# Performance work log

Hardware: AMD Instinct MI355X
Metric: run time of the kernel (lower is better)

## Reference

```python
import jax, jax.numpy as jnp
import numpy as np


def setup_inputs() -> dict:
    key = jax.random.key(0)
    k1, k2 = jax.random.split(key)
    BATCH, NUM_PROBES, DIM = 2048, 512, 256
    X = jax.random.uniform(k1, (BATCH, DIM), dtype=jnp.float32)
    probes = jax.random.uniform(k2, (NUM_PROBES, DIM), dtype=jnp.float32)
    return {"X": X, "probes": probes}


def reference(X, probes):
    # Godel implication a -> b: 1.0 if a <= b else b, applied on the
    # broadcast [batch, num_probes, dim] grid, then mean over dim.
    Xe = X[:, None, :]            # [B, 1, D]
    Pe = probes[None, :, :]       # [1, P, D]
    implication = jnp.where(Pe <= Xe, jnp.float32(1.0), Xe)  # [B, P, D]
    return implication.mean(axis=-1)  # [B, P]
```

## Files before the change

### kernel.cpp

```cpp
#include <hip/hip_runtime.h>
#include <stdint.h>


#define BATCH  2048
#define NPROBE 512
#define DIM    256

typedef float f4 __attribute__((ext_vector_type(4)));
typedef float f2 __attribute__((ext_vector_type(2)));

__global__ __launch_bounds__(1024, 4)
void yoneda_kernel(const float* __restrict__ X, const float* __restrict__ Pr,
                   float* __restrict__ out) {
  __shared__ float lds[32768];

  const int tid = threadIdx.x;
  const int b0 = blockIdx.y * 64, p0 = blockIdx.x * 64;
  const float K = 16777216.0f;

  #pragma unroll
  for (int s = 0; s < 4; ++s) {
    int idx = s * 1024 + tid;
    int r = idx >> 6, q = idx & 63;
    int slot = (q & 56) | ((q ^ r) & 7);
    f4 xv = *(const f4*)(X  + (size_t)(b0 + r) * DIM + 4 * q);
    f4 pv = *(const f4*)(Pr + (size_t)(p0 + r) * DIM + 4 * q);
    f4 yv, qv;
    #pragma unroll
    for (int e = 0; e < 4; ++e) {
      yv[e] = 1.0f - xv[e];
      qv[e] = __builtin_fmaf(pv[e], -K, K) + 1.0f;
    }
    *(f4*)&lds[r * 256 + 4 * slot]         = yv;
    *(f4*)&lds[16384 + r * 256 + 4 * slot] = qv;
  }

  const int wv   = tid >> 6;
  const int g2   = wv >> 1;
  const int ph   = wv & 1;
  const int gtid = tid & 63;
  const int tb   = gtid >> 3;
  const int tp   = gtid & 7;

  int xrow[8], prow[4];
  #pragma unroll
  for (int i = 0; i < 8; ++i) xrow[i] = (tb + 8 * i) * 256 + g2 * 32;
  #pragma unroll
  for (int j = 0; j < 4; ++j) prow[j] = 16384 + (ph * 32 + tp + 8 * j) * 256 + g2 * 32;

  f2 acc2[8][4], accy2[8];
  #pragma unroll
  for (int i = 0; i < 8; ++i) {
    accy2[i] = (f2){0.0f, 0.0f};
    #pragma unroll
    for (int j = 0; j < 4; ++j) acc2[i][j] = (f2){0.0f, 0.0f};
  }
  const f2 mK2 = {-K, -K};

  __syncthreads();

  #pragma unroll 1
  for (int s = 0; s < 8; ++s) {
    const int xo = 4 * (s ^ tb);
    const int po = 4 * (s ^ tp);
    f4 pv[4];
    #pragma unroll
    for (int j = 0; j < 4; ++j) pv[j] = *(const f4*)&lds[prow[j] + po];
    #pragma unroll
    for (int i = 0; i < 8; ++i) {
      f4 yv = *(const f4*)&lds[xrow[i] + xo];
      f2 ya = {yv[0], yv[1]}, yc = {yv[2], yv[3]};
      accy2[i] += ya;
      accy2[i] += yc;
      #pragma unroll
      for (int j = 0; j < 4; ++j) {
        f2 pa = {pv[j][0], pv[j][1]}, pc = {pv[j][2], pv[j][3]};
        f2 ma, mc;
        asm("v_pk_fma_f32 %0, %1, %2, %3 clamp"
            : "=v"(ma) : "v"(ya), "v"(mK2), "v"(pa));
        asm("v_pk_fma_f32 %0, %1, %2, %0"
            : "+v"(acc2[i][j]) : "v"(ma), "v"(ya));
        asm("v_pk_fma_f32 %0, %1, %2, %3 clamp"
            : "=v"(mc) : "v"(yc), "v"(mK2), "v"(pc));
        asm("v_pk_fma_f32 %0, %1, %2, %0"
            : "+v"(acc2[i][j]) : "v"(mc), "v"(yc));
      }
    }
  }

  __syncthreads();
  const int tbx   = tb << 2;
  const int obase = tb * 64 + ph * 32 + tp;
  const int gseg  = g2 << 12;
  #pragma unroll
  for (int i = 0; i < 8; ++i) {
    float sxg = 32.0f - (accy2[i][0] + accy2[i][1]);
    #pragma unroll
    for (int j = 0; j < 4; ++j) {
      int o = obase + 512 * i + 8 * j;
      lds[gseg + (o ^ tbx)] = sxg + acc2[i][j][0] + acc2[i][j][1];
    }
  }
  __syncthreads();
  const float inv  = 1.0f / 256.0f;
  const int   fold = ((tid >> 5) & 7) << 2;
  #pragma unroll
  for (int k = 0; k < 2; ++k) {
    int o = 2 * (k * 1024 + tid);
    int a = o ^ fold;
    f2 v = *(const f2*)&lds[a];
    #pragma unroll
    for (int g = 1; g < 8; ++g)
      v += *(const f2*)&lds[(g << 12) + a];
    v *= inv;
    int row = o >> 6, col = o & 63;
    *(f2*)&out[(size_t)(b0 + row) * NPROBE + p0 + col] = v;
  }
}

extern "C" void kernel_launch(void* const* d_in, const int* in_sizes, int n_in,
                              void* d_out, int out_size, void* d_ws, size_t ws_size,
                              hipStream_t stream) {
  const float* X  = (const float*)d_in[0];
  const float* Pr = (const float*)d_in[1];
  float* outp = (float*)d_out;
  dim3 grid(NPROBE / 64, BATCH / 64);
  yoneda_kernel<<<grid, 1024, 0, stream>>>(X, Pr, outp);
}
```

Baseline: 22.07 us.

## Split into prep kernel and main kernel using scalar-broadcast probe operands

```diff
diff --git a/kernel.cpp b/kernel.cpp
--- a/kernel.cpp
+++ b/kernel.cpp
@@ -9,15 +9,113 @@
 typedef float f4 __attribute__((ext_vector_type(4)));
 typedef float f2 __attribute__((ext_vector_type(2)));
 
+#define KF 16777216.0f
+#define Q1_OFF 0
+#define SX_OFF (NPROBE * DIM)
+#define WS_NEED ((size_t)((SX_OFF + BATCH) * 4))
+
+__global__ __launch_bounds__(512)
+void prep_kernel(const float* __restrict__ X, const float* __restrict__ Pr,
+                 float* __restrict__ ws) {
+  const int wv   = blockIdx.x * 8 + (threadIdx.x >> 6);
+  const int lane = threadIdx.x & 63;
+  if (wv < BATCH) {
+    f4 v = *(const f4*)(X + (size_t)wv * DIM + 4 * lane);
+    float s = (v[0] + v[1]) + (v[2] + v[3]);
+    #pragma unroll
+    for (int off = 32; off; off >>= 1) s += __shfl_xor(s, off, 64);
+    if (lane == 0) ws[SX_OFF + wv] = s;
+  } else {
+    const int p = wv - BATCH;
+    f4 v = *(const f4*)(Pr + (size_t)p * DIM + 4 * lane);
+    f4 q;
+    #pragma unroll
+    for (int e = 0; e < 4; ++e)
+      q[e] = __builtin_fmaf(v[e], -KF, KF) + 1.0f;
+    *(f4*)(ws + Q1_OFF + (size_t)p * DIM + 4 * lane) = q;
+  }
+}
+
+__global__ __launch_bounds__(512, 2)
+void yoneda_main(const float* __restrict__ X, const float* __restrict__ ws,
+                 float* __restrict__ out) {
+  __shared__ float yl[64 * 260];
+
+  const int tid = threadIdx.x;
+  const int p0  = blockIdx.x * 64;
+  const int b0  = blockIdx.y * 64;
+
+  #pragma unroll
+  for (int s = 0; s < 8; ++s) {
+    int idx = s * 512 + tid;
+    int r = idx >> 6, c = idx & 63;
+    f4 v = *(const f4*)(X + (size_t)(b0 + r) * DIM + 4 * c);
+    f4 y;
+    #pragma unroll
+    for (int e = 0; e < 4; ++e) y[e] = 1.0f - v[e];
+    *(f4*)&yl[r * 260 + 4 * c] = y;
+  }
+
+  const int w = __builtin_amdgcn_readfirstlane(tid >> 6);
+  const int l = tid & 63;
+  const float* q1w = ws + Q1_OFF + (size_t)(p0 + w * 8) * DIM;
+  const float sxv  = ws[SX_OFF + b0 + l];
+
+  f2 acc[8];
+  #pragma unroll
+  for (int j = 0; j < 8; ++j) acc[j] = (f2){0.0f, 0.0f};
+  const f2 mK2 = {-KF, -KF};
+
+  __syncthreads();
+
+  #pragma unroll 1
+  for (int dc = 0; dc < 4; ++dc) {
+    f4 yq[16];
+    #pragma unroll
+    for (int i = 0; i < 16; ++i)
+      yq[i] = *(const f4*)&yl[l * 260 + dc * 64 + 4 * i];
+    #pragma unroll
+    for (int jj = 0; jj < 8; ++jj) {
+      const f2* q2p = (const f2*)(q1w + jj * DIM + dc * 64);
+      #pragma unroll
+      for (int u = 0; u < 32; ++u) {
+        f2 q2 = q2p[u];
+        f2 y2 = (u & 1) ? (f2){yq[u >> 1][2], yq[u >> 1][3]}
+                        : (f2){yq[u >> 1][0], yq[u >> 1][1]};
+        f2 m;
+        asm("v_pk_fma_f32 %0, %1, %2, %3 clamp"
+            : "=v"(m) : "v"(y2), "v"(mK2), "s"(q2));
+        asm("v_pk_fma_f32 %0, %1, %2, %0"
+            : "+v"(acc[jj]) : "v"(m), "v"(y2));
+      }
+    }
+  }
+
+  __syncthreads();
+  #pragma unroll
+  for (int jj = 0; jj < 8; ++jj)
+    yl[(w * 8 + jj) * 65 + l] = sxv + (acc[jj][0] + acc[jj][1]);
+  __syncthreads();
+  const float inv = 1.0f / 256.0f;
+  const int r  = tid >> 3;
+  const int pb = (tid & 7) * 8;
+  f4 o0, o1;
+  #pragma unroll
+  for (int j = 0; j < 4; ++j) {
+    o0[j] = yl[(pb + j) * 65 + r] * inv;
+    o1[j] = yl[(pb + 4 + j) * 65 + r] * inv;
+  }
+  size_t ro = (size_t)(b0 + r) * NPROBE + p0 + pb;
+  *(f4*)(out + ro)     = o0;
+  *(f4*)(out + ro + 4) = o1;
+}
+
 __global__ __launch_bounds__(1024, 4)
-void yoneda_kernel(const float* __restrict__ X, const float* __restrict__ Pr,
-                   float* __restrict__ out) {
+void yoneda_fb(const float* __restrict__ X, const float* __restrict__ Pr,
+               float* __restrict__ out) {
   __shared__ float lds[32768];
-
   const int tid = threadIdx.x;
   const int b0 = blockIdx.y * 64, p0 = blockIdx.x * 64;
-  const float K = 16777216.0f;
-
   #pragma unroll
   for (int s = 0; s < 4; ++s) {
     int idx = s * 1024 + tid;
@@ -29,25 +127,18 @@
     #pragma unroll
     for (int e = 0; e < 4; ++e) {
       yv[e] = 1.0f - xv[e];
-      qv[e] = __builtin_fmaf(pv[e], -K, K) + 1.0f;
+      qv[e] = __builtin_fmaf(pv[e], -KF, KF) + 1.0f;
     }
     *(f4*)&lds[r * 256 + 4 * slot]         = yv;
     *(f4*)&lds[16384 + r * 256 + 4 * slot] = qv;
   }
-
-  const int wv   = tid >> 6;
-  const int g2   = wv >> 1;
-  const int ph   = wv & 1;
-  const int gtid = tid & 63;
-  const int tb   = gtid >> 3;
-  const int tp   = gtid & 7;
-
+  const int wv = tid >> 6, g2 = wv >> 1, ph = wv & 1;
+  const int gtid = tid & 63, tb = gtid >> 3, tp = gtid & 7;
   int xrow[8], prow[4];
   #pragma unroll
   for (int i = 0; i < 8; ++i) xrow[i] = (tb + 8 * i) * 256 + g2 * 32;
   #pragma unroll
   for (int j = 0; j < 4; ++j) prow[j] = 16384 + (ph * 32 + tp + 8 * j) * 256 + g2 * 32;
-
   f2 acc2[8][4], accy2[8];
   #pragma unroll
   for (int i = 0; i < 8; ++i) {
@@ -55,14 +146,11 @@
     #pragma unroll
     for (int j = 0; j < 4; ++j) acc2[i][j] = (f2){0.0f, 0.0f};
   }
-  const f2 mK2 = {-K, -K};
-
-  __syncthreads();
-
+  const f2 mK2 = {-KF, -KF};
+  __syncthreads();
   #pragma unroll 1
   for (int s = 0; s < 8; ++s) {
-    const int xo = 4 * (s ^ tb);
-    const int po = 4 * (s ^ tp);
+    const int xo = 4 * (s ^ tb), po = 4 * (s ^ tp);
     f4 pv[4];
     #pragma unroll
     for (int j = 0; j < 4; ++j) pv[j] = *(const f4*)&lds[prow[j] + po];
@@ -70,28 +158,20 @@
     for (int i = 0; i < 8; ++i) {
       f4 yv = *(const f4*)&lds[xrow[i] + xo];
       f2 ya = {yv[0], yv[1]}, yc = {yv[2], yv[3]};
-      accy2[i] += ya;
-      accy2[i] += yc;
+      accy2[i] += ya; accy2[i] += yc;
       #pragma unroll
       for (int j = 0; j < 4; ++j) {
         f2 pa = {pv[j][0], pv[j][1]}, pc = {pv[j][2], pv[j][3]};
         f2 ma, mc;
-        asm("v_pk_fma_f32 %0, %1, %2, %3 clamp"
-            : "=v"(ma) : "v"(ya), "v"(mK2), "v"(pa));
-        asm("v_pk_fma_f32 %0, %1, %2, %0"
-            : "+v"(acc2[i][j]) : "v"(ma), "v"(ya));
-        asm("v_pk_fma_f32 %0, %1, %2, %3 clamp"
-            : "=v"(mc) : "v"(yc), "v"(mK2), "v"(pc));
-        asm("v_pk_fma_f32 %0, %1, %2, %0"
-            : "+v"(acc2[i][j]) : "v"(mc), "v"(yc));
+        asm("v_pk_fma_f32 %0, %1, %2, %3 clamp" : "=v"(ma) : "v"(ya), "v"(mK2), "v"(pa));
+        asm("v_pk_fma_f32 %0, %1, %2, %0" : "+v"(acc2[i][j]) : "v"(ma), "v"(ya));
+        asm("v_pk_fma_f32 %0, %1, %2, %3 clamp" : "=v"(mc) : "v"(yc), "v"(mK2), "v"(pc));
+        asm("v_pk_fma_f32 %0, %1, %2, %0" : "+v"(acc2[i][j]) : "v"(mc), "v"(yc));
       }
     }
   }
-
-  __syncthreads();
-  const int tbx   = tb << 2;
-  const int obase = tb * 64 + ph * 32 + tp;
-  const int gseg  = g2 << 12;
+  __syncthreads();
+  const int tbx = tb << 2, obase = tb * 64 + ph * 32 + tp, gseg = g2 << 12;
   #pragma unroll
   for (int i = 0; i < 8; ++i) {
     float sxg = 32.0f - (accy2[i][0] + accy2[i][1]);
@@ -102,16 +182,15 @@
     }
   }
   __syncthreads();
-  const float inv  = 1.0f / 256.0f;
-  const int   fold = ((tid >> 5) & 7) << 2;
+  const float inv = 1.0f / 256.0f;
+  const int fold = ((tid >> 5) & 7) << 2;
   #pragma unroll
   for (int k = 0; k < 2; ++k) {
     int o = 2 * (k * 1024 + tid);
     int a = o ^ fold;
     f2 v = *(const f2*)&lds[a];
     #pragma unroll
-    for (int g = 1; g < 8; ++g)
-      v += *(const f2*)&lds[(g << 12) + a];
+    for (int g = 1; g < 8; ++g) v += *(const f2*)&lds[(g << 12) + a];
     v *= inv;
     int row = o >> 6, col = o & 63;
     *(f2*)&out[(size_t)(b0 + row) * NPROBE + p0 + col] = v;
@@ -124,6 +203,14 @@
   const float* X  = (const float*)d_in[0];
   const float* Pr = (const float*)d_in[1];
   float* outp = (float*)d_out;
-  dim3 grid(NPROBE / 64, BATCH / 64);
-  yoneda_kernel<<<grid, 1024, 0, stream>>>(X, Pr, outp);
-}
+
+  if (ws_size >= WS_NEED) {
+    float* ws = (float*)d_ws;
+    prep_kernel<<<320, 512, 0, stream>>>(X, Pr, ws);
+    dim3 grid(NPROBE / 64, BATCH / 64);
+    yoneda_main<<<grid, 512, 0, stream>>>(X, ws, outp);
+  } else {
+    dim3 grid(NPROBE / 64, BATCH / 64);
+    yoneda_fb<<<grid, 1024, 0, stream>>>(X, Pr, outp);
+  }
+}
```

New measurement: 41.70 us. 89.0% more time.

## Shrink tile to 64x32, stage X via direct global-to-LDS loads in two chunks

Applied to the files above, without the earlier changes.

```diff
diff --git a/kernel.cpp b/kernel.cpp
--- a/kernel.cpp
+++ b/kernel.cpp
@@ -5,48 +5,28 @@
 #define BATCH  2048
 #define NPROBE 512
 #define DIM    256
+#define KF 16777216.0f
 
 typedef float f4 __attribute__((ext_vector_type(4)));
 typedef float f2 __attribute__((ext_vector_type(2)));
 
-__global__ __launch_bounds__(1024, 4)
+static __device__ __forceinline__ void gl_lds16(const void* g, void* l) {
+  __builtin_amdgcn_global_load_lds(
+      (const __attribute__((address_space(1))) void*)g,
+      (__attribute__((address_space(3))) void*)l, 16, 0, 0);
+}
+
+__global__ __launch_bounds__(512, 4)
 void yoneda_kernel(const float* __restrict__ X, const float* __restrict__ Pr,
                    float* __restrict__ out) {
-  __shared__ float lds[32768];
+  __shared__ float lds[18688];
+  float* Ps = lds + 8192;
 
   const int tid = threadIdx.x;
-  const int b0 = blockIdx.y * 64, p0 = blockIdx.x * 64;
-  const float K = 16777216.0f;
-
-  #pragma unroll
-  for (int s = 0; s < 4; ++s) {
-    int idx = s * 1024 + tid;
-    int r = idx >> 6, q = idx & 63;
-    int slot = (q & 56) | ((q ^ r) & 7);
-    f4 xv = *(const f4*)(X  + (size_t)(b0 + r) * DIM + 4 * q);
-    f4 pv = *(const f4*)(Pr + (size_t)(p0 + r) * DIM + 4 * q);
-    f4 yv, qv;
-    #pragma unroll
-    for (int e = 0; e < 4; ++e) {
-      yv[e] = 1.0f - xv[e];
-      qv[e] = __builtin_fmaf(pv[e], -K, K) + 1.0f;
-    }
-    *(f4*)&lds[r * 256 + 4 * slot]         = yv;
-    *(f4*)&lds[16384 + r * 256 + 4 * slot] = qv;
-  }
-
-  const int wv   = tid >> 6;
-  const int g2   = wv >> 1;
-  const int ph   = wv & 1;
-  const int gtid = tid & 63;
-  const int tb   = gtid >> 3;
-  const int tp   = gtid & 7;
-
-  int xrow[8], prow[4];
-  #pragma unroll
-  for (int i = 0; i < 8; ++i) xrow[i] = (tb + 8 * i) * 256 + g2 * 32;
-  #pragma unroll
-  for (int j = 0; j < 4; ++j) prow[j] = 16384 + (ph * 32 + tp + 8 * j) * 256 + g2 * 32;
+  const int p0 = blockIdx.x * 32, b0 = blockIdx.y * 64;
+  const int w  = tid >> 6;
+  const int tb = (tid >> 3) & 7;
+  const int tp = tid & 7;
 
   f2 acc2[8][4], accy2[8];
   #pragma unroll
@@ -55,66 +35,82 @@
     #pragma unroll
     for (int j = 0; j < 4; ++j) acc2[i][j] = (f2){0.0f, 0.0f};
   }
-  const f2 mK2 = {-K, -K};
-
-  __syncthreads();
+  const f2 K2 = {KF, KF};
 
   #pragma unroll 1
-  for (int s = 0; s < 8; ++s) {
-    const int xo = 4 * (s ^ tb);
-    const int po = 4 * (s ^ tp);
-    f4 pv[4];
+  for (int c = 0; c < 2; ++c) {
     #pragma unroll
-    for (int j = 0; j < 4; ++j) pv[j] = *(const f4*)&lds[prow[j] + po];
+    for (int s = 0; s < 4; ++s) {
+      int idx = s * 512 + tid;
+      int r = idx >> 5, l = idx & 31;
+      gl_lds16(X + (size_t)(b0 + r) * DIM + c * 128 + 4 * (l ^ (r & 7)),
+               &lds[idx * 4]);
+    }
     #pragma unroll
-    for (int i = 0; i < 8; ++i) {
-      f4 yv = *(const f4*)&lds[xrow[i] + xo];
-      f2 ya = {yv[0], yv[1]}, yc = {yv[2], yv[3]};
-      accy2[i] += ya;
-      accy2[i] += yc;
+    for (int s = 0; s < 2; ++s) {
+      int idx = s * 512 + tid;
+      int r = idx >> 5, l = idx & 31;
+      f4 p = *(const f4*)(Pr + (size_t)(p0 + r) * DIM + c * 128 + 4 * l);
+      f4 q;
       #pragma unroll
-      for (int j = 0; j < 4; ++j) {
-        f2 pa = {pv[j][0], pv[j][1]}, pc = {pv[j][2], pv[j][3]};
-        f2 ma, mc;
-        asm("v_pk_fma_f32 %0, %1, %2, %3 clamp"
-            : "=v"(ma) : "v"(ya), "v"(mK2), "v"(pa));
-        asm("v_pk_fma_f32 %0, %1, %2, %0"
-            : "+v"(acc2[i][j]) : "v"(ma), "v"(ya));
-        asm("v_pk_fma_f32 %0, %1, %2, %3 clamp"
-            : "=v"(mc) : "v"(yc), "v"(mK2), "v"(pc));
-        asm("v_pk_fma_f32 %0, %1, %2, %0"
-            : "+v"(acc2[i][j]) : "v"(mc), "v"(yc));
+      for (int e = 0; e < 4; ++e) q[e] = __builtin_fmaf(p[e], -KF, 1.0f);
+      *(f4*)&Ps[(r * 32 + (l ^ (r & 7))) * 4] = q;
+    }
+    __syncthreads();
+
+    #pragma unroll
+    for (int s = 0; s < 4; ++s) {
+      const int l = w + 8 * s;
+      f4 pv[4];
+      #pragma unroll
+      for (int j = 0; j < 4; ++j)
+        pv[j] = *(const f4*)&Ps[((tp + 8 * j) * 32 + (l ^ tp)) * 4];
+      #pragma unroll
+      for (int i = 0; i < 8; ++i) {
+        f4 xv = *(const f4*)&lds[((tb + 8 * i) * 32 + (l ^ tb)) * 4];
+        f2 xa = {xv[0], xv[1]}, xc = {xv[2], xv[3]};
+        f2 ya = (f2){1.0f, 1.0f} - xa;
+        f2 yc = (f2){1.0f, 1.0f} - xc;
+        accy2[i] += ya;
+        accy2[i] += yc;
+        #pragma unroll
+        for (int j = 0; j < 4; ++j) {
+          f2 pa = {pv[j][0], pv[j][1]}, pc = {pv[j][2], pv[j][3]};
+          f2 ma, mc;
+          asm("v_pk_fma_f32 %0, %1, %2, %3 clamp"
+              : "=v"(ma) : "v"(xa), "v"(K2), "v"(pa));
+          asm("v_pk_fma_f32 %0, %1, %2, %0"
+              : "+v"(acc2[i][j]) : "v"(ma), "v"(ya));
+          asm("v_pk_fma_f32 %0, %1, %2, %3 clamp"
+              : "=v"(mc) : "v"(xc), "v"(K2), "v"(pc));
+          asm("v_pk_fma_f32 %0, %1, %2, %0"
+              : "+v"(acc2[i][j]) : "v"(mc), "v"(yc));
+        }
       }
     }
+    __syncthreads();
   }
 
-  __syncthreads();
-  const int tbx   = tb << 2;
-  const int obase = tb * 64 + ph * 32 + tp;
-  const int gseg  = g2 << 12;
   #pragma unroll
   for (int i = 0; i < 8; ++i) {
-    float sxg = 32.0f - (accy2[i][0] + accy2[i][1]);
+    float sxp = 32.0f - (accy2[i][0] + accy2[i][1]);
     #pragma unroll
     for (int j = 0; j < 4; ++j) {
-      int o = obase + 512 * i + 8 * j;
-      lds[gseg + (o ^ tbx)] = sxg + acc2[i][j][0] + acc2[i][j][1];
+      int row = tb + 8 * i, col = tp + 8 * j;
+      lds[row * 292 + col * 9 + w] = sxp + acc2[i][j][0] + acc2[i][j][1];
     }
   }
   __syncthreads();
-  const float inv  = 1.0f / 256.0f;
-  const int   fold = ((tid >> 5) & 7) << 2;
+  const float inv = 1.0f / 256.0f;
   #pragma unroll
-  for (int k = 0; k < 2; ++k) {
-    int o = 2 * (k * 1024 + tid);
-    int a = o ^ fold;
-    f2 v = *(const f2*)&lds[a];
+  for (int k = 0; k < 4; ++k) {
+    int o = tid + 512 * k;
+    int row = o >> 5, col = o & 31;
+    int base = row * 292 + col * 9;
+    float v = lds[base];
     #pragma unroll
-    for (int g = 1; g < 8; ++g)
-      v += *(const f2*)&lds[(g << 12) + a];
-    v *= inv;
-    int row = o >> 6, col = o & 63;
-    *(f2*)&out[(size_t)(b0 + row) * NPROBE + p0 + col] = v;
+    for (int g = 1; g < 8; ++g) v += lds[base + g];
+    out[(size_t)(b0 + row) * NPROBE + p0 + col] = v * inv;
   }
 }
 
@@ -124,6 +120,6 @@
   const float* X  = (const float*)d_in[0];
   const float* Pr = (const float*)d_in[1];
   float* outp = (float*)d_out;
-  dim3 grid(NPROBE / 64, BATCH / 64);
-  yoneda_kernel<<<grid, 1024, 0, stream>>>(X, Pr, outp);
+  dim3 grid(NPROBE / 32, BATCH / 64);
+  yoneda_kernel<<<grid, 512, 0, stream>>>(X, Pr, outp);
 }
```

Result: slower. 29.51 us (+33.7%).
